# Kernel tuning notes

Hardware: AMD Instinct MI355X
Metric: run time of the kernel (lower is better)

## Reference

```python
import jax, jax.numpy as jnp
import numpy as np

EP = 1e-4
MAX_ITER = 100
NEG = -1e9
H = 8


def _layernorm(x, g, b, eps=1e-5):
    m = jnp.mean(x, axis=-1, keepdims=True)
    v = jnp.mean((x - m) ** 2, axis=-1, keepdims=True)
    return (x - m) * jax.lax.rsqrt(v + eps) * g + b


def _nonsat(x):
    # Fixed-point iteration y_{n+1} = (2 y^3/3 + x)/(y^2 + 1); torch detaches y each
    # step, so gradient only flows through x in the final update.
    xs = jax.lax.stop_gradient(x)

    def step(y):
        y2 = y * y
        return (2.0 * y * y2 / 3.0 + xs) / (y2 + 1.0)

    def cond(st):
        y, yn, i = st
        return jnp.logical_and(jnp.mean(jnp.abs(yn - y)) > EP, i <= MAX_ITER)

    def body(st):
        y, yn, i = st
        return (yn, step(yn), i + 1)

    y_prev, _, _ = jax.lax.while_loop(cond, body, (xs, step(xs), jnp.int32(0)))
    y2 = y_prev * y_prev
    return (2.0 * y_prev * y2 / 3.0 + x) / (y2 + 1.0)


def setup_inputs() -> dict:
    key = jax.random.key(0)
    ks = jax.random.split(key, 20)
    S, B, E = 256, 64, 512
    DH, SW, DSS, DFF, DEPTH = 512, 64, 128, 2048, 32
    sd = 0.02
    inp = {
        'x_in': jax.random.normal(ks[0], (S, B, E), jnp.float32),
        'stack_prev': jax.random.normal(ks[1], (B, S, DEPTH, SW), jnp.float32),
        'k_mask': jnp.zeros((B, S), jnp.bool_),
        'ln1_g': jnp.ones((E,), jnp.float32),
        'ln1_b': jnp.zeros((E,), jnp.float32),
        'in_proj_w': jax.random.normal(ks[2], (E, 3 * E), jnp.float32) * sd,
        'in_proj_b': jnp.zeros((3 * E,), jnp.float32),
        'out_w': jax.random.normal(ks[3], (E, E), jnp.float32) * sd,
        'out_b': jnp.zeros((E,), jnp.float32),
        'W_w': jax.random.normal(ks[4], (E, DH), jnp.float32) * sd,
        'W_b': jnp.zeros((DH,), jnp.float32),
        'P_w': jax.random.normal(ks[5], (SW, DH), jnp.float32) * sd,
        'P_b': jnp.zeros((DH,), jnp.float32),
        'V_w': jax.random.normal(ks[6], (E + DH, DSS), jnp.float32) * sd,
        'U_w': jax.random.normal(ks[7], (DSS, E), jnp.float32) * sd,
        'A_w': jax.random.normal(ks[8], (DH, 3), jnp.float32) * sd,
        'A_b': jnp.zeros((3,), jnp.float32),
        'D_w': jax.random.normal(ks[9], (DH, SW), jnp.float32) * sd,
        'D_b': jnp.zeros((SW,), jnp.float32),
        'ln2_g': jnp.ones((E,), jnp.float32),
        'ln2_b': jnp.zeros((E,), jnp.float32),
        'ff1_w': jax.random.normal(ks[10], (E, DFF), jnp.float32) * sd,
        'ff1_b': jnp.zeros((DFF,), jnp.float32),
        'ff2_w': jax.random.normal(ks[11], (DFF, E), jnp.float32) * sd,
        'ff2_b': jnp.zeros((E,), jnp.float32),
    }
    return inp


def reference(x_in, stack_prev, k_mask, ln1_g, ln1_b, in_proj_w, in_proj_b, out_w,
              out_b, W_w, W_b, P_w, P_b, V_w, U_w, A_w, A_b, D_w, D_b, ln2_g,
              ln2_b, ff1_w, ff1_b, ff2_w, ff2_b):
    S, B, E = x_in.shape
    hd = E // H
    scale = 1.0 / np.sqrt(hd)

    # --- sublayer 0: pre-norm causal self-attention ---
    xn = _layernorm(x_in, ln1_g, ln1_b)
    qkv = xn @ in_proj_w + in_proj_b            # (S,B,3E)
    q, k, v = jnp.split(qkv, 3, axis=-1)
    q = q.reshape(S, B, H, hd)
    k = k.reshape(S, B, H, hd)
    v = v.reshape(S, B, H, hd)
    scores = jnp.einsum('sbhd,tbhd->bhst', q, k) * scale
    causal = jnp.triu(jnp.full((S, S), NEG, x_in.dtype), k=1)
    scores = scores + causal
    scores = jnp.where(k_mask[:, None, None, :], NEG, scores)
    attn = jax.nn.softmax(scores, axis=-1)
    ao = jnp.einsum('bhst,tbhd->sbhd', attn, v).reshape(S, B, E)
    x = x_in + ao @ out_w + out_b

    # --- stack-augmented memory ---
    stack_x = stack_prev[:, :, 0, :]            # (B,S,SW) top of stack
    xb = jnp.transpose(x, (1, 0, 2))            # (B,S,E)
    hidden = _nonsat(xb @ W_w + W_b + stack_x @ P_w + P_b)  # (B,S,DH)
    vx = jnp.concatenate([x, jnp.transpose(hidden, (1, 0, 2))], axis=-1)
    y = jax.nn.softmax(vx @ V_w, axis=-1) @ U_w
    x = jnp.maximum(x, y)

    stack_inp = _nonsat(hidden @ D_w + D_b)[:, :, None, :]   # (B,S,1,SW)
    ctrl = jax.nn.softmax(hidden @ A_w + A_b, axis=-1)[..., None, None]  # (B,S,3,1,1)
    zeros = jnp.zeros_like(stack_prev[:, :, :1])
    stack_down = jnp.concatenate([stack_prev[:, :, 1:], zeros], axis=2)
    stack_up = jnp.concatenate([stack_inp, stack_prev[:, :, :-1]], axis=2)
    stack = ctrl[:, :, 2] * stack_prev + ctrl[:, :, 0] * stack_up + ctrl[:, :, 1] * stack_down

    # --- sublayer 1: pre-norm FFN ---
    xn2 = _layernorm(x, ln2_g, ln2_b)
    x = x + jax.nn.relu(xn2 @ ff1_w + ff1_b) @ ff2_w + ff2_b
    return (x, stack)
```

## Files before the change

### kernel.cpp

```cpp
#include <hip/hip_runtime.h>
#include <math.h>

#define S_DIM 256
#define B_DIM 64
#define E_DIM 512
#define H_NUM 8
#define HD 64
#define DH 512
#define SW 64
#define DSS 128
#define DFF 2048
#define DEPTH 32
#define M_ROWS 16384

typedef __attribute__((ext_vector_type(8))) short bf16x8;
typedef __attribute__((ext_vector_type(4))) float f32x4;

__device__ __forceinline__ ushort f2bf(float v){
    unsigned int u = __float_as_uint(v);
    u += 0x7fffu + ((u >> 16) & 1u);
    return (ushort)(u >> 16);
}
__device__ __forceinline__ float bf2f(ushort s){
    return __uint_as_float(((unsigned int)s) << 16);
}
__device__ __forceinline__ void splitbf(float v, ushort& h, ushort& l){
    h = f2bf(v);
    l = f2bf(v - bf2f(h));
}

__device__ __forceinline__ int perm32(int k){
    return ((k >> 2) & 3) * 8 + (k & 3) + ((k >> 4) << 2);
}

__device__ __forceinline__ float nonsat_f(float x){
    float y = x;
#pragma unroll
    for (int i = 0; i < 10; i++){
        float y2 = y * y;
        y = (0.66666666f * y * y2 + x) / (y2 + 1.0f);
    }
    return y;
}

__global__ __launch_bounds__(256) void ln_split(const float* __restrict__ x,
                                                const float* __restrict__ g,
                                                const float* __restrict__ bta,
                                                ushort* __restrict__ oh,
                                                ushort* __restrict__ ol){
    __shared__ float red[4];
    int r = blockIdx.x;
    int t = threadIdx.x;
    const float* xr = x + (size_t)r * E_DIM;
    float v0 = xr[t], v1 = xr[t + 256];
    float s = v0 + v1;
#pragma unroll
    for (int off = 32; off > 0; off >>= 1) s += __shfl_xor(s, off, 64);
    if ((t & 63) == 0) red[t >> 6] = s;
    __syncthreads();
    float mean = (red[0] + red[1] + red[2] + red[3]) * (1.0f / 512.0f);
    __syncthreads();
    float d0 = v0 - mean, d1 = v1 - mean;
    float q = d0 * d0 + d1 * d1;
#pragma unroll
    for (int off = 32; off > 0; off >>= 1) q += __shfl_xor(q, off, 64);
    if ((t & 63) == 0) red[t >> 6] = q;
    __syncthreads();
    float var = (red[0] + red[1] + red[2] + red[3]) * (1.0f / 512.0f);
    float rs = rsqrtf(var + 1e-5f);
    size_t base = (size_t)r * E_DIM;
    float y0 = d0 * rs * g[t]       + bta[t];
    float y1 = d1 * rs * g[t + 256] + bta[t + 256];
    int pc = (t & ~31) | perm32(t & 31);
    ushort h, l;
    splitbf(y0, h, l); oh[base + pc] = h;       ol[base + pc] = l;
    splitbf(y1, h, l); oh[base + pc + 256] = h; ol[base + pc + 256] = l;
}

__global__ __launch_bounds__(256) void wsplit_t(const float* __restrict__ W,
                                                ushort* __restrict__ th,
                                                ushort* __restrict__ tl,
                                                int K, int N, int Ktot, int koff){
    __shared__ float tile[32][33];
    int n0 = blockIdx.x << 5, k0 = blockIdx.y << 5;
    int tx = threadIdx.x & 31, ty = threadIdx.x >> 5;
#pragma unroll
    for (int i = 0; i < 32; i += 8)
        tile[ty + i][tx] = W[(size_t)(k0 + ty + i) * N + (n0 + tx)];
    __syncthreads();
    int pk = perm32(tx);
#pragma unroll
    for (int i = 0; i < 32; i += 8){
        int n = ty + i;
        float v = tile[tx][n];
        ushort h, l; splitbf(v, h, l);
        th[(size_t)(n0 + n) * Ktot + koff + k0 + pk] = h;
        tl[(size_t)(n0 + n) * Ktot + koff + k0 + pk] = l;
    }
}

__global__ __launch_bounds__(256) void build_dab(const float* __restrict__ Dw,
                                                 const float* __restrict__ Db,
                                                 const float* __restrict__ Aw,
                                                 const float* __restrict__ Ab,
                                                 const float* __restrict__ Wb,
                                                 const float* __restrict__ Pb,
                                                 float* __restrict__ DA,
                                                 float* __restrict__ dabb,
                                                 float* __restrict__ hbias){
    int idx = blockIdx.x * 256 + threadIdx.x;
    if (idx < 65536){
        int k = idx >> 7, c = idx & 127;
        float v = 0.f;
        if (c < 64) v = Dw[k * 64 + c];
        else if (c < 67) v = Aw[k * 3 + (c - 64)];
        DA[idx] = v;
    }
    if (idx < 128){
        float v = 0.f;
        if (idx < 64) v = Db[idx];
        else if (idx < 67) v = Ab[idx - 64];
        dabb[idx] = v;
    }
    if (idx < 512) hbias[idx] = Wb[idx] + Pb[idx];
}

__global__ __launch_bounds__(256) void gemm_bf3(
    const ushort* __restrict__ Ah, const ushort* __restrict__ Al,
    const ushort* __restrict__ Bh, const ushort* __restrict__ Bl,
    const float* __restrict__ bias, const float* __restrict__ res,
    float* __restrict__ Cf, ushort* __restrict__ Ch, ushort* __restrict__ Cl,
    int M, int N, int K, int act, int resmode)
{
    __shared__ __align__(16) ushort lds[20480];
    const int tid = threadIdx.x;
    int lin = blockIdx.y * gridDim.x + blockIdx.x;
    int nloc = (gridDim.x * gridDim.y) >> 3;
    int id = (lin & 7) * nloc + (lin >> 3);
    const int n0 = (id % gridDim.x) << 7, m0 = (id / gridDim.x) << 7;

    const int srow = tid >> 2, schunk = tid & 3;
    const int sOff = srow * 40 + (schunk << 3);
    const ushort* gA0 = Ah + (size_t)(m0 + srow) * K + (schunk << 3);
    const ushort* gA1 = Al + (size_t)(m0 + srow) * K + (schunk << 3);
    const ushort* gB0 = Bh + (size_t)(n0 + srow) * K + (schunk << 3);
    const ushort* gB1 = Bl + (size_t)(n0 + srow) * K + (schunk << 3);
    const size_t rstep = (size_t)64 * K;

    const int lane = tid & 63;
    const int wv = tid >> 6;
    const int wm = (wv >> 1) << 6, wn = (wv & 1) << 6;
    const int r0 = lane & 15, gq = lane >> 4;

    f32x4 acc[4][4];
    f32x4 zero = {0.f, 0.f, 0.f, 0.f};
#pragma unroll
    for (int i = 0; i < 4; i++)
#pragma unroll
        for (int j = 0; j < 4; j++) acc[i][j] = zero;

    uint4 v0,v1,v2,v3,v4,v5,v6,v7;
    v0 = *(const uint4*)(gA0);          v1 = *(const uint4*)(gA0 + rstep);
    v2 = *(const uint4*)(gA1);          v3 = *(const uint4*)(gA1 + rstep);
    v4 = *(const uint4*)(gB0);          v5 = *(const uint4*)(gB0 + rstep);
    v6 = *(const uint4*)(gB1);          v7 = *(const uint4*)(gB1 + rstep);

    for (int k0 = 0; k0 < K; k0 += 32){
        __syncthreads();
        *(uint4*)(&lds[sOff])                = v0;
        *(uint4*)(&lds[sOff + 2560])         = v1;
        *(uint4*)(&lds[5120 + sOff])         = v2;
        *(uint4*)(&lds[5120 + sOff + 2560])  = v3;
        *(uint4*)(&lds[10240 + sOff])        = v4;
        *(uint4*)(&lds[10240 + sOff + 2560]) = v5;
        *(uint4*)(&lds[15360 + sOff])        = v6;
        *(uint4*)(&lds[15360 + sOff + 2560]) = v7;
        __syncthreads();
        if (k0 + 32 < K){
            gA0 += 32; gA1 += 32; gB0 += 32; gB1 += 32;
            v0 = *(const uint4*)(gA0);  v1 = *(const uint4*)(gA0 + rstep);
            v2 = *(const uint4*)(gA1);  v3 = *(const uint4*)(gA1 + rstep);
            v4 = *(const uint4*)(gB0);  v5 = *(const uint4*)(gB0 + rstep);
            v6 = *(const uint4*)(gB1);  v7 = *(const uint4*)(gB1 + rstep);
        }
        bf16x8 fa[4], fal[4];
#pragma unroll
        for (int fr = 0; fr < 4; fr++){
            int off = (wm + (fr << 4) + r0) * 40 + (gq << 3);
            fa[fr]  = *(const bf16x8*)(&lds[off]);
            fal[fr] = *(const bf16x8*)(&lds[off + 5120]);
        }
#pragma unroll
        for (int fc = 0; fc < 4; fc++){
            int off = (wn + (fc << 4) + r0) * 40 + (gq << 3);
            bf16x8 fbh = *(const bf16x8*)(&lds[off + 10240]);
            bf16x8 fbl = *(const bf16x8*)(&lds[off + 15360]);
#pragma unroll
            for (int fr = 0; fr < 4; fr++){
                acc[fr][fc] = __builtin_amdgcn_mfma_f32_16x16x32_bf16(fa[fr],  fbh, acc[fr][fc], 0, 0, 0);
                acc[fr][fc] = __builtin_amdgcn_mfma_f32_16x16x32_bf16(fa[fr],  fbl, acc[fr][fc], 0, 0, 0);
                acc[fr][fc] = __builtin_amdgcn_mfma_f32_16x16x32_bf16(fal[fr], fbh, acc[fr][fc], 0, 0, 0);
            }
        }
    }
#pragma unroll
    for (int fc = 0; fc < 4; fc++){
        int col = n0 + wn + (fc << 4) + r0;
        int pcol = (col & ~31) | perm32(col & 31);
        float bc = bias ? bias[col] : 0.f;
#pragma unroll
        for (int fr = 0; fr < 4; fr++){
#pragma unroll
            for (int e = 0; e < 4; e++){
                int row = m0 + wm + (fr << 4) + (gq << 2) + e;
                size_t idx = (size_t)row * N + col;
                float v = acc[fr][fc][e] + bc;
                if (resmode == 1) v += res[idx];
                else if (resmode == 2) v = fmaxf(v, res[idx]);
                if (act == 1) v = fmaxf(v, 0.f);
                else if (act == 2) v = nonsat_f(v);
                if (Cf) Cf[idx] = v;
                if (Ch){
                    ushort hh, ll; splitbf(v, hh, ll);
                    size_t pidx = (size_t)row * N + pcol;
                    Ch[pidx] = hh; Cl[pidx] = ll;
                }
            }
        }
    }
}

__global__ __launch_bounds__(256) void gemm_hidden_bf3(
    const ushort* __restrict__ x1h, const ushort* __restrict__ x1l,
    const float* __restrict__ stack_prev,
    const ushort* __restrict__ Bh, const ushort* __restrict__ Bl,
    const float* __restrict__ bias,
    float* __restrict__ hidden)
{
    __shared__ __align__(16) ushort lds[20480];
    const int tid = threadIdx.x;
    int lin = blockIdx.y * gridDim.x + blockIdx.x;
    int nloc = (gridDim.x * gridDim.y) >> 3;
    int id = (lin & 7) * nloc + (lin >> 3);
    const int n0 = (id % gridDim.x) << 7, m0 = (id / gridDim.x) << 7;

    const int srow = tid >> 2, schunk = tid & 3;
    const int sOff = srow * 40 + (schunk << 3);
    const int ra = m0 + srow, rb = m0 + 64 + srow;
    const int xra = ((ra & 255) << 6) | (ra >> 8);
    const int xrb = ((rb & 255) << 6) | (rb >> 8);
    const ushort* gB0 = Bh + (size_t)(n0 + srow) * 576 + (schunk << 3);
    const ushort* gB1 = Bl + (size_t)(n0 + srow) * 576 + (schunk << 3);
    const size_t rstepB = (size_t)64 * 576;

    const int lane = tid & 63;
    const int wv = tid >> 6;
    const int wm = (wv >> 1) << 6, wn = (wv & 1) << 6;
    const int r0 = lane & 15, gq = lane >> 4;

    auto fetchA = [&](int k0, int row, int xr, uint4& vh, uint4& vl){
        if (k0 < 512){
            vh = *(const uint4*)(x1h + (size_t)xr * 512 + k0 + (schunk << 3));
            vl = *(const uint4*)(x1l + (size_t)xr * 512 + k0 + (schunk << 3));
        } else {
            const float* sp = stack_prev + (size_t)row * 2048 + (k0 - 512) + (schunk << 2);
            float f[8];
            *(float4*)(f)     = *(const float4*)(sp);
            *(float4*)(f + 4) = *(const float4*)(sp + 16);
            union { ushort us[8]; uint4 u4; } th, tl;
#pragma unroll
            for (int j = 0; j < 8; j++) splitbf(f[j], th.us[j], tl.us[j]);
            vh = th.u4; vl = tl.u4;
        }
    };

    f32x4 acc[4][4];
    f32x4 zero = {0.f, 0.f, 0.f, 0.f};
#pragma unroll
    for (int i = 0; i < 4; i++)
#pragma unroll
        for (int j = 0; j < 4; j++) acc[i][j] = zero;

    uint4 v0,v1,v2,v3,v4,v5,v6,v7;
    fetchA(0, ra, xra, v0, v2);
    fetchA(0, rb, xrb, v1, v3);
    v4 = *(const uint4*)(gB0); v5 = *(const uint4*)(gB0 + rstepB);
    v6 = *(const uint4*)(gB1); v7 = *(const uint4*)(gB1 + rstepB);

    for (int k0 = 0; k0 < 576; k0 += 32){
        __syncthreads();
        *(uint4*)(&lds[sOff])                = v0;
        *(uint4*)(&lds[sOff + 2560])         = v1;
        *(uint4*)(&lds[5120 + sOff])         = v2;
        *(uint4*)(&lds[5120 + sOff + 2560])  = v3;
        *(uint4*)(&lds[10240 + sOff])        = v4;
        *(uint4*)(&lds[10240 + sOff + 2560]) = v5;
        *(uint4*)(&lds[15360 + sOff])        = v6;
        *(uint4*)(&lds[15360 + sOff + 2560]) = v7;
        __syncthreads();
        if (k0 + 32 < 576){
            fetchA(k0 + 32, ra, xra, v0, v2);
            fetchA(k0 + 32, rb, xrb, v1, v3);
            gB0 += 32; gB1 += 32;
            v4 = *(const uint4*)(gB0); v5 = *(const uint4*)(gB0 + rstepB);
            v6 = *(const uint4*)(gB1); v7 = *(const uint4*)(gB1 + rstepB);
        }
        bf16x8 fa[4], fal[4];
#pragma unroll
        for (int fr = 0; fr < 4; fr++){
            int off = (wm + (fr << 4) + r0) * 40 + (gq << 3);
            fa[fr]  = *(const bf16x8*)(&lds[off]);
            fal[fr] = *(const bf16x8*)(&lds[off + 5120]);
        }
#pragma unroll
        for (int fc = 0; fc < 4; fc++){
            int off = (wn + (fc << 4) + r0) * 40 + (gq << 3);
            bf16x8 fbh = *(const bf16x8*)(&lds[off + 10240]);
            bf16x8 fbl = *(const bf16x8*)(&lds[off + 15360]);
#pragma unroll
            for (int fr = 0; fr < 4; fr++){
                acc[fr][fc] = __builtin_amdgcn_mfma_f32_16x16x32_bf16(fa[fr],  fbh, acc[fr][fc], 0, 0, 0);
                acc[fr][fc] = __builtin_amdgcn_mfma_f32_16x16x32_bf16(fa[fr],  fbl, acc[fr][fc], 0, 0, 0);
                acc[fr][fc] = __builtin_amdgcn_mfma_f32_16x16x32_bf16(fal[fr], fbh, acc[fr][fc], 0, 0, 0);
            }
        }
    }
#pragma unroll
    for (int fc = 0; fc < 4; fc++){
        int col = n0 + wn + (fc << 4) + r0;
        float bc = bias[col];
#pragma unroll
        for (int fr = 0; fr < 4; fr++){
#pragma unroll
            for (int e = 0; e < 4; e++){
                int row = m0 + wm + (fr << 4) + (gq << 2) + e;
                hidden[(size_t)row * 512 + col] = nonsat_f(acc[fr][fc][e] + bc);
            }
        }
    }
}

__global__ __launch_bounds__(256) void gemm_k(const float* __restrict__ A,
                                              const float* __restrict__ W,
                                              const float* __restrict__ bias,
                                              const float* __restrict__ res,
                                              float* __restrict__ C,
                                              int M, int N, int K,
                                              int act, int resmode){
    __shared__ float As[32][68];
    __shared__ float Ws[32][68];
    int m0 = blockIdx.x << 6, n0 = blockIdx.y << 6;
    int tid = threadIdx.x;
    int tx = tid & 15, ty = tid >> 4;
    float acc[4][4] = {{0.f}};
    for (int k0 = 0; k0 < K; k0 += 32){
#pragma unroll
        for (int i = 0; i < 8; i++){
            int e = tid + (i << 8);
            int row = e >> 5, col = e & 31;
            As[col][row] = A[(size_t)(m0 + row) * K + (k0 + col)];
        }
#pragma unroll
        for (int i = 0; i < 8; i++){
            int e = tid + (i << 8);
            int kk = e >> 6, nn = e & 63;
            Ws[kk][nn] = W[(size_t)(k0 + kk) * N + (n0 + nn)];
        }
        __syncthreads();
#pragma unroll
        for (int kk = 0; kk < 32; kk++){
            float4 a = *(const float4*)(&As[kk][ty << 2]);
            float4 b = *(const float4*)(&Ws[kk][tx << 2]);
            float av[4] = {a.x, a.y, a.z, a.w};
            float bv[4] = {b.x, b.y, b.z, b.w};
#pragma unroll
            for (int i = 0; i < 4; i++)
#pragma unroll
                for (int j = 0; j < 4; j++) acc[i][j] = fmaf(av[i], bv[j], acc[i][j]);
        }
        __syncthreads();
    }
    int nbase = n0 + (tx << 2);
    float4 bv4 = make_float4(0.f, 0.f, 0.f, 0.f);
    if (bias) bv4 = *(const float4*)(bias + nbase);
#pragma unroll
    for (int i = 0; i < 4; i++){
        int mm = m0 + (ty << 2) + i;
        size_t idx = (size_t)mm * N + nbase;
        float v0 = acc[i][0] + bv4.x, v1 = acc[i][1] + bv4.y;
        float v2 = acc[i][2] + bv4.z, v3 = acc[i][3] + bv4.w;
        if (resmode == 1){
            float4 rv = *(const float4*)(res + idx);
            v0 += rv.x; v1 += rv.y; v2 += rv.z; v3 += rv.w;
        } else if (resmode == 2){
            float4 rv = *(const float4*)(res + idx);
            v0 = fmaxf(v0, rv.x); v1 = fmaxf(v1, rv.y);
            v2 = fmaxf(v2, rv.z); v3 = fmaxf(v3, rv.w);
        }
        if (act == 1){
            v0 = fmaxf(v0, 0.f); v1 = fmaxf(v1, 0.f);
            v2 = fmaxf(v2, 0.f); v3 = fmaxf(v3, 0.f);
        }
        *(float4*)(C + idx) = make_float4(v0, v1, v2, v3);
    }
}

__global__ __launch_bounds__(256) void gemm_vx(const float* __restrict__ x1,
                                               const float* __restrict__ hidden,
                                               const float* __restrict__ Vw,
                                               float* __restrict__ t){
    __shared__ float As[32][68];
    __shared__ float Ws[32][68];
    int m0 = blockIdx.x << 6, n0 = blockIdx.y << 6;
    int tid = threadIdx.x;
    int tx = tid & 15, ty = tid >> 4;
    float acc[4][4] = {{0.f}};
    for (int k0 = 0; k0 < 1024; k0 += 32){
        if (k0 < 512){
#pragma unroll
            for (int i = 0; i < 8; i++){
                int e = tid + (i << 8);
                int row = e >> 5, col = e & 31;
                As[col][row] = x1[(size_t)(m0 + row) * 512 + (k0 + col)];
            }
        } else {
#pragma unroll
            for (int i = 0; i < 8; i++){
                int e = tid + (i << 8);
                int row = e >> 5, col = e & 31;
                int r = m0 + row;
                int hr = ((r & 63) << 8) | (r >> 6);
                As[col][row] = hidden[(size_t)hr * 512 + (k0 - 512 + col)];
            }
        }
#pragma unroll
        for (int i = 0; i < 8; i++){
            int e = tid + (i << 8);
            int kk = e >> 6, nn = e & 63;
            Ws[kk][nn] = Vw[(size_t)(k0 + kk) * 128 + (n0 + nn)];
        }
        __syncthreads();
#pragma unroll
        for (int kk = 0; kk < 32; kk++){
            float4 a = *(const float4*)(&As[kk][ty << 2]);
            float4 b = *(const float4*)(&Ws[kk][tx << 2]);
            float av[4] = {a.x, a.y, a.z, a.w};
            float bv[4] = {b.x, b.y, b.z, b.w};
#pragma unroll
            for (int i = 0; i < 4; i++)
#pragma unroll
                for (int j = 0; j < 4; j++) acc[i][j] = fmaf(av[i], bv[j], acc[i][j]);
        }
        __syncthreads();
    }
    int nbase = n0 + (tx << 2);
#pragma unroll
    for (int i = 0; i < 4; i++){
        int mm = m0 + (ty << 2) + i;
        *(float4*)(t + (size_t)mm * 128 + nbase) =
            make_float4(acc[i][0], acc[i][1], acc[i][2], acc[i][3]);
    }
}

__global__ __launch_bounds__(128) void softmax128(float* __restrict__ t){
    __shared__ float red[2];
    int r = blockIdx.x, c = threadIdx.x;
    float v = t[(size_t)r * 128 + c];
    float m = v;
#pragma unroll
    for (int off = 32; off > 0; off >>= 1) m = fmaxf(m, __shfl_xor(m, off, 64));
    if ((c & 63) == 0) red[c >> 6] = m;
    __syncthreads();
    m = fmaxf(red[0], red[1]);
    __syncthreads();
    float e = expf(v - m);
    float s = e;
#pragma unroll
    for (int off = 32; off > 0; off >>= 1) s += __shfl_xor(s, off, 64);
    if ((c & 63) == 0) red[c >> 6] = s;
    __syncthreads();
    s = red[0] + red[1];
    t[(size_t)r * 128 + c] = e / s;
}

__global__ __launch_bounds__(256) void attn_kernel(const float* __restrict__ qkv,
                                                   ushort* __restrict__ aoh,
                                                   ushort* __restrict__ aol){
    __shared__ float Qs[64 * 68];
    __shared__ float KV[64 * 68];
    __shared__ float Ps[64 * 68];
    int bid = blockIdx.x;
    int ti = bid & 3, h = (bid >> 2) & 7, b = bid >> 5;
    int tid = threadIdx.x;
    int tx = tid & 15, ty = tid >> 4;
    const float scale = 0.125f;

    {
        const float* qbase = qkv + (size_t)b * 1536 + (h << 6);
#pragma unroll
        for (int i = 0; i < 4; i++){
            int f4 = tid + (i << 8);
            int r = f4 >> 4, c4 = f4 & 15;
            *(float4*)(&Qs[r * 68 + (c4 << 2)]) =
                *(const float4*)(qbase + (size_t)(((ti << 6) + r) << 6) * 1536 + (c4 << 2));
        }
    }
    float m_i[4], l_i[4], O[4][4];
#pragma unroll
    for (int i = 0; i < 4; i++){
        m_i[i] = -1e30f; l_i[i] = 0.f;
#pragma unroll
        for (int j = 0; j < 4; j++) O[i][j] = 0.f;
    }

    for (int tk = 0; tk <= ti; tk++){
        __syncthreads();
        {
            const float* kbase = qkv + (size_t)b * 1536 + 512 + (h << 6);
#pragma unroll
            for (int i = 0; i < 4; i++){
                int f4 = tid + (i << 8);
                int r = f4 >> 4, c4 = f4 & 15;
                *(float4*)(&KV[(r << 6) + (((c4 ^ (r >> 2)) & 15) << 2)]) =
                    *(const float4*)(kbase + (size_t)(((tk << 6) + r) << 6) * 1536 + (c4 << 2));
            }
        }
        __syncthreads();
        float sv[4][4] = {{0.f}};
#pragma unroll
        for (int d4 = 0; d4 < 16; d4++){
            float4 qa[4], kb[4];
#pragma unroll
            for (int i = 0; i < 4; i++)
                qa[i] = *(const float4*)(&Qs[((ty << 2) + i) * 68 + (d4 << 2)]);
#pragma unroll
            for (int j = 0; j < 4; j++)
                kb[j] = *(const float4*)(&KV[(((tx << 2) + j) << 6) + (((d4 ^ tx) & 15) << 2)]);
#pragma unroll
            for (int i = 0; i < 4; i++)
#pragma unroll
                for (int j = 0; j < 4; j++){
                    sv[i][j] = fmaf(qa[i].x, kb[j].x, sv[i][j]);
                    sv[i][j] = fmaf(qa[i].y, kb[j].y, sv[i][j]);
                    sv[i][j] = fmaf(qa[i].z, kb[j].z, sv[i][j]);
                    sv[i][j] = fmaf(qa[i].w, kb[j].w, sv[i][j]);
                }
        }
#pragma unroll
        for (int i = 0; i < 4; i++)
#pragma unroll
            for (int j = 0; j < 4; j++){
                float v = sv[i][j] * scale;
                if (tk == ti && ((tx << 2) + j) > ((ty << 2) + i)) v = -1e30f;
                sv[i][j] = v;
            }
        float alpha[4];
#pragma unroll
        for (int i = 0; i < 4; i++){
            float rm = fmaxf(fmaxf(sv[i][0], sv[i][1]), fmaxf(sv[i][2], sv[i][3]));
#pragma unroll
            for (int off = 8; off > 0; off >>= 1) rm = fmaxf(rm, __shfl_xor(rm, off, 64));
            float mn = fmaxf(m_i[i], rm);
            alpha[i] = __expf(m_i[i] - mn);
            float rs = 0.f;
#pragma unroll
            for (int j = 0; j < 4; j++){
                sv[i][j] = __expf(sv[i][j] - mn);
                rs += sv[i][j];
            }
#pragma unroll
            for (int off = 8; off > 0; off >>= 1) rs += __shfl_xor(rs, off, 64);
            l_i[i] = l_i[i] * alpha[i] + rs;
            m_i[i] = mn;
        }
#pragma unroll
        for (int i = 0; i < 4; i++)
            *(float4*)(&Ps[((ty << 2) + i) * 68 + (tx << 2)]) =
                make_float4(sv[i][0], sv[i][1], sv[i][2], sv[i][3]);
        __syncthreads();
        {
            const float* vbase = qkv + (size_t)b * 1536 + 1024 + (h << 6);
#pragma unroll
            for (int i = 0; i < 4; i++){
                int f4 = tid + (i << 8);
                int r = f4 >> 4, c4 = f4 & 15;
                *(float4*)(&KV[r * 68 + (c4 << 2)]) =
                    *(const float4*)(vbase + (size_t)(((tk << 6) + r) << 6) * 1536 + (c4 << 2));
            }
        }
        __syncthreads();
#pragma unroll
        for (int i = 0; i < 4; i++)
#pragma unroll
            for (int j = 0; j < 4; j++) O[i][j] *= alpha[i];
#pragma unroll
        for (int t4 = 0; t4 < 16; t4++){
            float4 pa[4], vb[4];
#pragma unroll
            for (int i = 0; i < 4; i++)
                pa[i] = *(const float4*)(&Ps[((ty << 2) + i) * 68 + (t4 << 2)]);
#pragma unroll
            for (int tt = 0; tt < 4; tt++)
                vb[tt] = *(const float4*)(&KV[((t4 << 2) + tt) * 68 + (tx << 2)]);
#pragma unroll
            for (int i = 0; i < 4; i++){
                float pav[4] = {pa[i].x, pa[i].y, pa[i].z, pa[i].w};
#pragma unroll
                for (int tt = 0; tt < 4; tt++){
                    O[i][0] = fmaf(pav[tt], vb[tt].x, O[i][0]);
                    O[i][1] = fmaf(pav[tt], vb[tt].y, O[i][1]);
                    O[i][2] = fmaf(pav[tt], vb[tt].z, O[i][2]);
                    O[i][3] = fmaf(pav[tt], vb[tt].w, O[i][3]);
                }
            }
        }
    }
#pragma unroll
    for (int i = 0; i < 4; i++){
        float inv = 1.0f / l_i[i];
        int sglob = (ti << 6) + (ty << 2) + i;
        int col = (h << 6) + (tx << 2);
        int pcol = (col & ~31) | perm32(col & 31);
        size_t idx = (size_t)((sglob << 6) + b) * 512 + pcol;
        ushort4 hv, lv;
        float o0 = O[i][0] * inv, o1 = O[i][1] * inv, o2 = O[i][2] * inv, o3 = O[i][3] * inv;
        splitbf(o0, hv.x, lv.x);
        splitbf(o1, hv.y, lv.y);
        splitbf(o2, hv.z, lv.z);
        splitbf(o3, hv.w, lv.w);
        *(ushort4*)(aoh + idx) = hv;
        *(ushort4*)(aol + idx) = lv;
    }
}

__global__ __launch_bounds__(256) void stack_update(const float* __restrict__ head,
                                                    const float* __restrict__ stack_prev,
                                                    float* __restrict__ stack_out){
    __shared__ float sinp[64];
    __shared__ float ctrl[3];
    int r = blockIdx.x;
    int tid = threadIdx.x;
    const float* hrow = head + (size_t)r * 128;
    if (tid < 64){
        sinp[tid] = nonsat_f(hrow[tid]);
    } else if (tid == 64){
        float a0 = hrow[64], a1 = hrow[65], a2 = hrow[66];
        float mx = fmaxf(a0, fmaxf(a1, a2));
        float e0 = expf(a0 - mx), e1 = expf(a1 - mx), e2 = expf(a2 - mx);
        float inv = 1.f / (e0 + e1 + e2);
        ctrl[0] = e0 * inv; ctrl[1] = e1 * inv; ctrl[2] = e2 * inv;
    }
    __syncthreads();
    float c0 = ctrl[0], c1 = ctrl[1], c2 = ctrl[2];
    const float* prow = stack_prev + (size_t)r * 2048;
    float* orow = stack_out + (size_t)r * 2048;
#pragma unroll
    for (int i = 0; i < 8; i++){
        int idx = tid + (i << 8);
        int dep = idx >> 6, j = idx & 63;
        float prev = prow[idx];
        float up   = dep ? prow[idx - 64] : sinp[j];
        float down = (dep < 31) ? prow[idx + 64] : 0.f;
        orow[idx] = c2 * prev + c0 * up + c1 * down;
    }
}

extern "C" void kernel_launch(void* const* d_in, const int* in_sizes, int n_in,
                              void* d_out, int out_size, void* d_ws, size_t ws_size,
                              hipStream_t stream){
    const float* x_in       = (const float*)d_in[0];
    const float* stack_prev = (const float*)d_in[1];
    const float* ln1_g = (const float*)d_in[3];
    const float* ln1_b = (const float*)d_in[4];
    const float* in_proj_w = (const float*)d_in[5];
    const float* in_proj_b = (const float*)d_in[6];
    const float* out_w = (const float*)d_in[7];
    const float* out_b = (const float*)d_in[8];
    const float* W_w = (const float*)d_in[9];
    const float* W_b = (const float*)d_in[10];
    const float* P_w = (const float*)d_in[11];
    const float* P_b = (const float*)d_in[12];
    const float* V_w = (const float*)d_in[13];
    const float* U_w = (const float*)d_in[14];
    const float* A_w = (const float*)d_in[15];
    const float* A_b = (const float*)d_in[16];
    const float* D_w = (const float*)d_in[17];
    const float* D_b = (const float*)d_in[18];
    const float* ln2_g = (const float*)d_in[19];
    const float* ln2_b = (const float*)d_in[20];
    const float* ff1_w = (const float*)d_in[21];
    const float* ff1_b = (const float*)d_in[22];
    const float* ff2_w = (const float*)d_in[23];
    const float* ff2_b = (const float*)d_in[24];

    float* dout_x     = (float*)d_out;
    float* dout_stack = dout_x + 8388608;
    float* qkv = dout_stack;
    float* x1  = dout_stack + 25165824;
    ushort* x1h = (ushort*)dout_stack;
    ushort* x1l = x1h + 8388608;
    ushort* fmh = (ushort*)(dout_stack + 8388608);
    ushort* fml = fmh + 16777216;

    float* ws   = (float*)d_ws;
    float* bufA = ws;
    float* x2   = ws + 8388608;
    float* tbuf = ws + 16777216;
    ushort* xnh = (ushort*)(ws + 18874368);
    ushort* xnl = xnh + 8388608;
    ushort* wb0 = (ushort*)(ws + 27262976);
    ushort* ipTh = wb0;
    ushort* ipTl = ipTh + 786432;
    ushort* owTh = ipTl + 786432;
    ushort* owTl = owTh + 262144;
    ushort* f1Th = owTl + 262144;
    ushort* f1Tl = f1Th + 1048576;
    ushort* f2Th = f1Tl + 1048576;
    ushort* f2Tl = f2Th + 1048576;
    ushort* whT  = f2Tl + 1048576;
    ushort* wlT  = whT + 294912;
    float* headbuf = ws + 30703616;
    float* DAw   = ws + 32800768;
    float* dabb  = ws + 32866304;
    float* hbias = ws + 32866432;

    wsplit_t<<<dim3(48, 16), 256, 0, stream>>>(in_proj_w, ipTh, ipTl, 512, 1536, 512, 0);
    wsplit_t<<<dim3(16, 16), 256, 0, stream>>>(out_w, owTh, owTl, 512, 512, 512, 0);
    wsplit_t<<<dim3(64, 16), 256, 0, stream>>>(ff1_w, f1Th, f1Tl, 512, 2048, 512, 0);
    wsplit_t<<<dim3(16, 64), 256, 0, stream>>>(ff2_w, f2Th, f2Tl, 2048, 512, 2048, 0);
    wsplit_t<<<dim3(16, 16), 256, 0, stream>>>(W_w, whT, wlT, 512, 512, 576, 0);
    wsplit_t<<<dim3(16, 2), 256, 0, stream>>>(P_w, whT, wlT, 64, 512, 576, 512);
    build_dab<<<256, 256, 0, stream>>>(D_w, D_b, A_w, A_b, W_b, P_b, DAw, dabb, hbias);

    ln_split<<<16384, 256, 0, stream>>>(x_in, ln1_g, ln1_b, xnh, xnl);
    gemm_bf3<<<dim3(12, 128), 256, 0, stream>>>(xnh, xnl, ipTh, ipTl, in_proj_b, nullptr,
                                                qkv, nullptr, nullptr, 16384, 1536, 512, 0, 0);
    attn_kernel<<<2048, 256, 0, stream>>>(qkv, xnh, xnl);
    gemm_bf3<<<dim3(4, 128), 256, 0, stream>>>(xnh, xnl, owTh, owTl, out_b, x_in,
                                               x1, x1h, x1l, 16384, 512, 512, 0, 1);
    gemm_hidden_bf3<<<dim3(4, 128), 256, 0, stream>>>(x1h, x1l, stack_prev, whT, wlT,
                                                      hbias, bufA);
    gemm_k<<<dim3(256, 2), 256, 0, stream>>>(bufA, DAw, dabb, nullptr, headbuf,
                                             16384, 128, 512, 0, 0);
    gemm_vx<<<dim3(256, 2), 256, 0, stream>>>(x1, bufA, V_w, tbuf);
    softmax128<<<16384, 128, 0, stream>>>(tbuf);
    gemm_k<<<dim3(256, 8), 256, 0, stream>>>(tbuf, U_w, nullptr, x1, x2,
                                             16384, 512, 128, 0, 2);
    ln_split<<<16384, 256, 0, stream>>>(x2, ln2_g, ln2_b, xnh, xnl);
    for (int c = 0; c < 2; c++){
        gemm_bf3<<<dim3(16, 64), 256, 0, stream>>>(xnh + c * 4194304, xnl + c * 4194304,
                                                   f1Th, f1Tl, ff1_b, nullptr,
                                                   nullptr, fmh, fml, 8192, 2048, 512, 1, 0);
        gemm_bf3<<<dim3(4, 64), 256, 0, stream>>>(fmh, fml, f2Th, f2Tl, ff2_b,
                                                  x2 + c * 4194304, dout_x + c * 4194304,
                                                  nullptr, nullptr, 8192, 512, 2048, 0, 1);
    }
    stack_update<<<16384, 256, 0, stream>>>(headbuf, stack_prev, dout_stack);
}
```

Before: 1.358 ms.

## Move attention to bf16x3 MFMA with transposed V and split QKV output

The QKV GEMM now writes high/low bf16 halves instead of fp32. A new vt_split kernel transposes V into a per-head layout, and the fp32 FMA flash-attention kernel is replaced by an MFMA version that uses three-product bf16 splitting for QK^T and PV. The online softmax now runs in registers with wave shuffles rather than through shared memory. The stack_update kernel is also vectorised to float4. The cost is an extra transpose kernel plus reliance on the column permutation layout matching the GEMM output, and split-bf16 precision is slightly lower than fp32.

```diff
diff --git a/kernel.cpp b/kernel.cpp
--- a/kernel.cpp
+++ b/kernel.cpp
@@ -31,6 +31,9 @@
 
 __device__ __forceinline__ int perm32(int k){
     return ((k >> 2) & 3) * 8 + (k & 3) + ((k >> 4) << 2);
+}
+__device__ __forceinline__ int iperm32(int p){
+    return (((p >> 2) & 1) << 4) | ((p >> 3) << 2) | (p & 3);
 }
 
 __device__ __forceinline__ float nonsat_f(float x){
@@ -483,160 +486,172 @@
     t[(size_t)r * 128 + c] = e / s;
 }
 
-__global__ __launch_bounds__(256) void attn_kernel(const float* __restrict__ qkv,
-                                                   ushort* __restrict__ aoh,
-                                                   ushort* __restrict__ aol){
-    __shared__ float Qs[64 * 68];
-    __shared__ float KV[64 * 68];
-    __shared__ float Ps[64 * 68];
+__global__ __launch_bounds__(256) void vt_split(const ushort* __restrict__ qkvh,
+                                                const ushort* __restrict__ qkvl,
+                                                ushort* __restrict__ vTh,
+                                                ushort* __restrict__ vTl){
+    __shared__ ushort lh[4096], ll[4096];
+    int bh = blockIdx.x; int b = bh >> 3, h = bh & 7;
+    int tt = blockIdx.y;
+    int tid = threadIdx.x;
+    int s = tid >> 2, c = tid & 3;
+    size_t rbase = ((size_t)((((tt << 6) + s) << 6) + b)) * 1536 + 1024 + (h << 6);
+    *(uint4*)(&lh[(s << 6) + (c << 3)])       = *(const uint4*)(qkvh + rbase + (c << 3));
+    *(uint4*)(&lh[(s << 6) + ((c + 4) << 3)]) = *(const uint4*)(qkvh + rbase + ((c + 4) << 3));
+    *(uint4*)(&ll[(s << 6) + (c << 3)])       = *(const uint4*)(qkvl + rbase + (c << 3));
+    *(uint4*)(&ll[(s << 6) + ((c + 4) << 3)]) = *(const uint4*)(qkvl + rbase + ((c + 4) << 3));
+    __syncthreads();
+    int d = tid >> 2;
+    int pc = (d & 32) | perm32(d & 31);
+#pragma unroll
+    for (int cc = 0; cc < 8; cc += 4){
+        int oc = (tid & 3) + cc;
+        union { ushort us[8]; uint4 u4; } oh, ol;
+#pragma unroll
+        for (int i = 0; i < 8; i++){
+            int p = (oc << 3) + i;
+            int tl_ = (p & 32) | iperm32(p & 31);
+            oh.us[i] = lh[(tl_ << 6) + pc];
+            ol.us[i] = ll[(tl_ << 6) + pc];
+        }
+        size_t obase = ((size_t)bh << 14) + ((size_t)d << 8) + (tt << 6) + (oc << 3);
+        *(uint4*)(vTh + obase) = oh.u4;
+        *(uint4*)(vTl + obase) = ol.u4;
+    }
+}
+
+__global__ __launch_bounds__(256) void attn_mfma(
+    const ushort* __restrict__ qkvh, const ushort* __restrict__ qkvl,
+    const ushort* __restrict__ vTh, const ushort* __restrict__ vTl,
+    ushort* __restrict__ aoh, ushort* __restrict__ aol)
+{
     int bid = blockIdx.x;
     int ti = bid & 3, h = (bid >> 2) & 7, b = bid >> 5;
     int tid = threadIdx.x;
-    int tx = tid & 15, ty = tid >> 4;
+    int w = tid >> 6;
+    int lane = tid & 63;
+    int r0 = lane & 15, gq = lane >> 4;
     const float scale = 0.125f;
 
-    {
-        const float* qbase = qkv + (size_t)b * 1536 + (h << 6);
-#pragma unroll
-        for (int i = 0; i < 4; i++){
-            int f4 = tid + (i << 8);
-            int r = f4 >> 4, c4 = f4 & 15;
-            *(float4*)(&Qs[r * 68 + (c4 << 2)]) =
-                *(const float4*)(qbase + (size_t)(((ti << 6) + r) << 6) * 1536 + (c4 << 2));
-        }
-    }
-    float m_i[4], l_i[4], O[4][4];
-#pragma unroll
-    for (int i = 0; i < 4; i++){
-        m_i[i] = -1e30f; l_i[i] = 0.f;
-#pragma unroll
-        for (int j = 0; j < 4; j++) O[i][j] = 0.f;
-    }
+    int qrow = ((((ti << 6) + (w << 4) + r0)) << 6) + b;
+    size_t qoff = (size_t)qrow * 1536 + (h << 6) + (gq << 3);
+    bf16x8 qh0 = *(const bf16x8*)(qkvh + qoff);
+    bf16x8 qh1 = *(const bf16x8*)(qkvh + qoff + 32);
+    bf16x8 ql0 = *(const bf16x8*)(qkvl + qoff);
+    bf16x8 ql1 = *(const bf16x8*)(qkvl + qoff + 32);
+
+    float m_i = -1e30f, l_i = 0.f;
+    f32x4 accO[4];
+    f32x4 zero = {0.f, 0.f, 0.f, 0.f};
+#pragma unroll
+    for (int fc = 0; fc < 4; fc++) accO[fc] = zero;
+
+    size_t vbb = (((size_t)((b << 3) + h)) << 14) + (gq << 3);
 
     for (int tk = 0; tk <= ti; tk++){
-        __syncthreads();
-        {
-            const float* kbase = qkv + (size_t)b * 1536 + 512 + (h << 6);
-#pragma unroll
-            for (int i = 0; i < 4; i++){
-                int f4 = tid + (i << 8);
-                int r = f4 >> 4, c4 = f4 & 15;
-                *(float4*)(&KV[(r << 6) + (((c4 ^ (r >> 2)) & 15) << 2)]) =
-                    *(const float4*)(kbase + (size_t)(((tk << 6) + r) << 6) * 1536 + (c4 << 2));
-            }
-        }
-        __syncthreads();
-        float sv[4][4] = {{0.f}};
-#pragma unroll
-        for (int d4 = 0; d4 < 16; d4++){
-            float4 qa[4], kb[4];
-#pragma unroll
-            for (int i = 0; i < 4; i++)
-                qa[i] = *(const float4*)(&Qs[((ty << 2) + i) * 68 + (d4 << 2)]);
-#pragma unroll
-            for (int j = 0; j < 4; j++)
-                kb[j] = *(const float4*)(&KV[(((tx << 2) + j) << 6) + (((d4 ^ tx) & 15) << 2)]);
-#pragma unroll
-            for (int i = 0; i < 4; i++)
-#pragma unroll
-                for (int j = 0; j < 4; j++){
-                    sv[i][j] = fmaf(qa[i].x, kb[j].x, sv[i][j]);
-                    sv[i][j] = fmaf(qa[i].y, kb[j].y, sv[i][j]);
-                    sv[i][j] = fmaf(qa[i].z, kb[j].z, sv[i][j]);
-                    sv[i][j] = fmaf(qa[i].w, kb[j].w, sv[i][j]);
+        f32x4 acc_s[4];
+#pragma unroll
+        for (int fr = 0; fr < 4; fr++) acc_s[fr] = zero;
+#pragma unroll
+        for (int fr = 0; fr < 4; fr++){
+            int krow = ((((tk << 6) + (fr << 4) + r0)) << 6) + b;
+            size_t kb = (size_t)krow * 1536 + 512 + (h << 6) + (gq << 3);
+            bf16x8 kh0 = *(const bf16x8*)(qkvh + kb);
+            bf16x8 kh1 = *(const bf16x8*)(qkvh + kb + 32);
+            bf16x8 kl0 = *(const bf16x8*)(qkvl + kb);
+            bf16x8 kl1 = *(const bf16x8*)(qkvl + kb + 32);
+            acc_s[fr] = __builtin_amdgcn_mfma_f32_16x16x32_bf16(kh0, qh0, acc_s[fr], 0, 0, 0);
+            acc_s[fr] = __builtin_amdgcn_mfma_f32_16x16x32_bf16(kh0, ql0, acc_s[fr], 0, 0, 0);
+            acc_s[fr] = __builtin_amdgcn_mfma_f32_16x16x32_bf16(kl0, qh0, acc_s[fr], 0, 0, 0);
+            acc_s[fr] = __builtin_amdgcn_mfma_f32_16x16x32_bf16(kh1, qh1, acc_s[fr], 0, 0, 0);
+            acc_s[fr] = __builtin_amdgcn_mfma_f32_16x16x32_bf16(kh1, ql1, acc_s[fr], 0, 0, 0);
+            acc_s[fr] = __builtin_amdgcn_mfma_f32_16x16x32_bf16(kl1, qh1, acc_s[fr], 0, 0, 0);
+        }
+        float p[4][4];
+        float pm = -1e30f;
+#pragma unroll
+        for (int fr = 0; fr < 4; fr++)
+#pragma unroll
+            for (int e = 0; e < 4; e++){
+                float v = acc_s[fr][e] * scale;
+                if (tk == ti){
+                    int tg = (fr << 4) + (gq << 2) + e;
+                    int qg = (w << 4) + r0;
+                    if (tg > qg) v = -1e30f;
                 }
-        }
-#pragma unroll
-        for (int i = 0; i < 4; i++)
-#pragma unroll
-            for (int j = 0; j < 4; j++){
-                float v = sv[i][j] * scale;
-                if (tk == ti && ((tx << 2) + j) > ((ty << 2) + i)) v = -1e30f;
-                sv[i][j] = v;
-            }
-        float alpha[4];
-#pragma unroll
-        for (int i = 0; i < 4; i++){
-            float rm = fmaxf(fmaxf(sv[i][0], sv[i][1]), fmaxf(sv[i][2], sv[i][3]));
-#pragma unroll
-            for (int off = 8; off > 0; off >>= 1) rm = fmaxf(rm, __shfl_xor(rm, off, 64));
-            float mn = fmaxf(m_i[i], rm);
-            alpha[i] = __expf(m_i[i] - mn);
-            float rs = 0.f;
-#pragma unroll
-            for (int j = 0; j < 4; j++){
-                sv[i][j] = __expf(sv[i][j] - mn);
-                rs += sv[i][j];
-            }
-#pragma unroll
-            for (int off = 8; off > 0; off >>= 1) rs += __shfl_xor(rs, off, 64);
-            l_i[i] = l_i[i] * alpha[i] + rs;
-            m_i[i] = mn;
-        }
-#pragma unroll
-        for (int i = 0; i < 4; i++)
-            *(float4*)(&Ps[((ty << 2) + i) * 68 + (tx << 2)]) =
-                make_float4(sv[i][0], sv[i][1], sv[i][2], sv[i][3]);
-        __syncthreads();
-        {
-            const float* vbase = qkv + (size_t)b * 1536 + 1024 + (h << 6);
-#pragma unroll
-            for (int i = 0; i < 4; i++){
-                int f4 = tid + (i << 8);
-                int r = f4 >> 4, c4 = f4 & 15;
-                *(float4*)(&KV[r * 68 + (c4 << 2)]) =
-                    *(const float4*)(vbase + (size_t)(((tk << 6) + r) << 6) * 1536 + (c4 << 2));
-            }
-        }
-        __syncthreads();
-#pragma unroll
-        for (int i = 0; i < 4; i++)
-#pragma unroll
-            for (int j = 0; j < 4; j++) O[i][j] *= alpha[i];
-#pragma unroll
-        for (int t4 = 0; t4 < 16; t4++){
-            float4 pa[4], vb[4];
-#pragma unroll
-            for (int i = 0; i < 4; i++)
-                pa[i] = *(const float4*)(&Ps[((ty << 2) + i) * 68 + (t4 << 2)]);
-#pragma unroll
-            for (int tt = 0; tt < 4; tt++)
-                vb[tt] = *(const float4*)(&KV[((t4 << 2) + tt) * 68 + (tx << 2)]);
-#pragma unroll
-            for (int i = 0; i < 4; i++){
-                float pav[4] = {pa[i].x, pa[i].y, pa[i].z, pa[i].w};
-#pragma unroll
-                for (int tt = 0; tt < 4; tt++){
-                    O[i][0] = fmaf(pav[tt], vb[tt].x, O[i][0]);
-                    O[i][1] = fmaf(pav[tt], vb[tt].y, O[i][1]);
-                    O[i][2] = fmaf(pav[tt], vb[tt].z, O[i][2]);
-                    O[i][3] = fmaf(pav[tt], vb[tt].w, O[i][3]);
-                }
-            }
-        }
-    }
-#pragma unroll
-    for (int i = 0; i < 4; i++){
-        float inv = 1.0f / l_i[i];
-        int sglob = (ti << 6) + (ty << 2) + i;
-        int col = (h << 6) + (tx << 2);
+                p[fr][e] = v;
+                pm = fmaxf(pm, v);
+            }
+        pm = fmaxf(pm, __shfl_xor(pm, 16, 64));
+        pm = fmaxf(pm, __shfl_xor(pm, 32, 64));
+        float mn = fmaxf(m_i, pm);
+        float alpha = __expf(m_i - mn);
+        float rs = 0.f;
+#pragma unroll
+        for (int fr = 0; fr < 4; fr++)
+#pragma unroll
+            for (int e = 0; e < 4; e++){
+                float pe = __expf(p[fr][e] - mn);
+                p[fr][e] = pe;
+                rs += pe;
+            }
+        rs += __shfl_xor(rs, 16, 64);
+        rs += __shfl_xor(rs, 32, 64);
+        l_i = l_i * alpha + rs;
+        m_i = mn;
+        float alq[4];
+#pragma unroll
+        for (int e = 0; e < 4; e++)
+            alq[e] = __shfl(alpha, (lane & 48) + (gq << 2) + e, 64);
+#pragma unroll
+        for (int fc = 0; fc < 4; fc++)
+#pragma unroll
+            for (int e = 0; e < 4; e++) accO[fc][e] *= alq[e];
+#pragma unroll
+        for (int ks = 0; ks < 2; ks++){
+            union { ushort us[8]; bf16x8 v; } pah, pal;
+#pragma unroll
+            for (int e = 0; e < 4; e++){
+                ushort hh, ll;
+                splitbf(p[2 * ks][e], hh, ll);
+                pah.us[e] = hh; pal.us[e] = ll;
+                splitbf(p[2 * ks + 1][e], hh, ll);
+                pah.us[4 + e] = hh; pal.us[4 + e] = ll;
+            }
+#pragma unroll
+            for (int fc = 0; fc < 4; fc++){
+                size_t va = vbb + ((size_t)((fc << 4) + r0) << 8) + (tk << 6) + (ks << 5);
+                bf16x8 vh = *(const bf16x8*)(vTh + va);
+                bf16x8 vl = *(const bf16x8*)(vTl + va);
+                accO[fc] = __builtin_amdgcn_mfma_f32_16x16x32_bf16(pah.v, vh, accO[fc], 0, 0, 0);
+                accO[fc] = __builtin_amdgcn_mfma_f32_16x16x32_bf16(pah.v, vl, accO[fc], 0, 0, 0);
+                accO[fc] = __builtin_amdgcn_mfma_f32_16x16x32_bf16(pal.v, vh, accO[fc], 0, 0, 0);
+            }
+        }
+    }
+    float inv[4];
+#pragma unroll
+    for (int e = 0; e < 4; e++)
+        inv[e] = 1.0f / __shfl(l_i, (lane & 48) + (gq << 2) + e, 64);
+#pragma unroll
+    for (int fc = 0; fc < 4; fc++){
+        int col = (h << 6) + (fc << 4) + r0;
         int pcol = (col & ~31) | perm32(col & 31);
-        size_t idx = (size_t)((sglob << 6) + b) * 512 + pcol;
-        ushort4 hv, lv;
-        float o0 = O[i][0] * inv, o1 = O[i][1] * inv, o2 = O[i][2] * inv, o3 = O[i][3] * inv;
-        splitbf(o0, hv.x, lv.x);
-        splitbf(o1, hv.y, lv.y);
-        splitbf(o2, hv.z, lv.z);
-        splitbf(o3, hv.w, lv.w);
-        *(ushort4*)(aoh + idx) = hv;
-        *(ushort4*)(aol + idx) = lv;
+#pragma unroll
+        for (int e = 0; e < 4; e++){
+            int s = (ti << 6) + (w << 4) + (gq << 2) + e;
+            size_t idx = (size_t)((s << 6) + b) * 512 + pcol;
+            float o = accO[fc][e] * inv[e];
+            ushort hh, ll; splitbf(o, hh, ll);
+            aoh[idx] = hh; aol[idx] = ll;
+        }
     }
 }
 
 __global__ __launch_bounds__(256) void stack_update(const float* __restrict__ head,
                                                     const float* __restrict__ stack_prev,
                                                     float* __restrict__ stack_out){
-    __shared__ float sinp[64];
+    __shared__ __align__(16) float sinp[64];
     __shared__ float ctrl[3];
     int r = blockIdx.x;
     int tid = threadIdx.x;
@@ -647,21 +662,27 @@
         float a0 = hrow[64], a1 = hrow[65], a2 = hrow[66];
         float mx = fmaxf(a0, fmaxf(a1, a2));
         float e0 = expf(a0 - mx), e1 = expf(a1 - mx), e2 = expf(a2 - mx);
-        float inv = 1.f / (e0 + e1 + e2);
-        ctrl[0] = e0 * inv; ctrl[1] = e1 * inv; ctrl[2] = e2 * inv;
+        float iv = 1.f / (e0 + e1 + e2);
+        ctrl[0] = e0 * iv; ctrl[1] = e1 * iv; ctrl[2] = e2 * iv;
     }
     __syncthreads();
     float c0 = ctrl[0], c1 = ctrl[1], c2 = ctrl[2];
-    const float* prow = stack_prev + (size_t)r * 2048;
-    float* orow = stack_out + (size_t)r * 2048;
-#pragma unroll
-    for (int i = 0; i < 8; i++){
+    const float4* prow = (const float4*)(stack_prev + (size_t)r * 2048);
+    float4* orow = (float4*)(stack_out + (size_t)r * 2048);
+    const float4* s4 = (const float4*)sinp;
+#pragma unroll
+    for (int i = 0; i < 2; i++){
         int idx = tid + (i << 8);
-        int dep = idx >> 6, j = idx & 63;
-        float prev = prow[idx];
-        float up   = dep ? prow[idx - 64] : sinp[j];
-        float down = (dep < 31) ? prow[idx + 64] : 0.f;
-        orow[idx] = c2 * prev + c0 * up + c1 * down;
+        int dep = idx >> 4;
+        float4 prev = prow[idx];
+        float4 up   = dep ? prow[idx - 16] : s4[idx & 15];
+        float4 down = (dep < 31) ? prow[idx + 16] : make_float4(0.f, 0.f, 0.f, 0.f);
+        float4 o;
+        o.x = c2 * prev.x + c0 * up.x + c1 * down.x;
+        o.y = c2 * prev.y + c0 * up.y + c1 * down.y;
+        o.z = c2 * prev.z + c0 * up.z + c1 * down.z;
+        o.w = c2 * prev.w + c0 * up.w + c1 * down.w;
+        orow[idx] = o;
     }
 }
 
@@ -695,12 +716,15 @@
 
     float* dout_x     = (float*)d_out;
     float* dout_stack = dout_x + 8388608;
-    float* qkv = dout_stack;
-    float* x1  = dout_stack + 25165824;
-    ushort* x1h = (ushort*)dout_stack;
-    ushort* x1l = x1h + 8388608;
-    ushort* fmh = (ushort*)(dout_stack + 8388608);
-    ushort* fml = fmh + 16777216;
+    ushort* qkvh = (ushort*)dout_stack;
+    ushort* qkvl = qkvh + 25165824;
+    ushort* vTh  = (ushort*)(dout_stack + 25165824);
+    ushort* vTl  = vTh + 8388608;
+    float*  x1   = dout_stack + 25165824;
+    ushort* x1h  = (ushort*)dout_stack;
+    ushort* x1l  = x1h + 8388608;
+    ushort* fmh  = (ushort*)(dout_stack + 8388608);
+    ushort* fml  = fmh + 16777216;
 
     float* ws   = (float*)d_ws;
     float* bufA = ws;
@@ -734,8 +758,9 @@
 
     ln_split<<<16384, 256, 0, stream>>>(x_in, ln1_g, ln1_b, xnh, xnl);
     gemm_bf3<<<dim3(12, 128), 256, 0, stream>>>(xnh, xnl, ipTh, ipTl, in_proj_b, nullptr,
-                                                qkv, nullptr, nullptr, 16384, 1536, 512, 0, 0);
-    attn_kernel<<<2048, 256, 0, stream>>>(qkv, xnh, xnl);
+                                                nullptr, qkvh, qkvl, 16384, 1536, 512, 0, 0);
+    vt_split<<<dim3(512, 4), 256, 0, stream>>>(qkvh, qkvl, vTh, vTl);
+    attn_mfma<<<2048, 256, 0, stream>>>(qkvh, qkvl, vTh, vTl, xnh, xnl);
     gemm_bf3<<<dim3(4, 128), 256, 0, stream>>>(xnh, xnl, owTh, owTl, out_b, x_in,
                                                x1, x1h, x1l, 16384, 512, 512, 0, 1);
     gemm_hidden_bf3<<<dim3(4, 128), 256, 0, stream>>>(x1h, x1l, stack_prev, whT, wlT,
```

Result: slower. 1.467 ms (+8.0%).
